# Kernel tuning notes

Hardware: AMD Instinct MI355X
Metric: run time of the kernel (lower is better)

Reference implementation:

```python
import jax, jax.numpy as jnp
import numpy as np

THRESHOLD = 0.5
NEG_POS_RATIO = 3
ALPHA = 10.0
N_PRIORS = 8732
N_CLASSES = 21
BATCH = 128
N_OBJ = 32


def cxcy_to_xy(cxcy):
    return jnp.concatenate([cxcy[..., :2] - cxcy[..., 2:] / 2.0,
                            cxcy[..., :2] + cxcy[..., 2:] / 2.0], axis=-1)


def xy_to_cxcy(xy):
    return jnp.concatenate([(xy[..., :2] + xy[..., 2:]) / 2.0,
                            xy[..., 2:] - xy[..., :2]], axis=-1)


def cxcy_to_gcxgcy(cxcy, priors_cxcy):
    return jnp.concatenate([(cxcy[..., :2] - priors_cxcy[..., :2]) / (priors_cxcy[..., 2:] / 10.0),
                            jnp.log(cxcy[..., 2:] / priors_cxcy[..., 2:]) * 5.0], axis=-1)


def find_jaccard_overlap(a, b):
    # a: (M,4) xyxy, b: (P,4) xyxy -> (M,P)
    lt = jnp.maximum(a[:, None, :2], b[None, :, :2])
    rb = jnp.minimum(a[:, None, 2:], b[None, :, 2:])
    wh = jnp.clip(rb - lt, 0.0)
    inter = wh[..., 0] * wh[..., 1]
    area_a = (a[:, 2] - a[:, 0]) * (a[:, 3] - a[:, 1])
    area_b = (b[:, 2] - b[:, 0]) * (b[:, 3] - b[:, 1])
    return inter / (area_a[:, None] + area_b[None, :] - inter)


def _match_one(boxes, labels, priors_xy, priors_cxcy):
    # boxes: (M,4) xyxy, labels: (M,)
    iou = find_jaccard_overlap(boxes, priors_xy)           # (M,P)
    obj_idx = jnp.argmax(iou, axis=1)                      # best prior per object
    iou = iou.at[jnp.arange(boxes.shape[0]), obj_idx].set(1.0)
    positive = (iou >= THRESHOLD).any(axis=0)              # (P,)
    max_prior_idx = jnp.argmax(iou, axis=0)                # best object per prior
    true_cls = labels[max_prior_idx] * positive.astype(labels.dtype)
    matched = boxes[max_prior_idx]                         # (P,4)
    true_locs = cxcy_to_gcxgcy(xy_to_cxcy(matched), priors_cxcy)
    return true_locs, true_cls, positive


def setup_inputs() -> dict:
    key = jax.random.key(0)
    k1, k2, k3, k4, k5, k6 = jax.random.split(key, 6)
    pred_loc = jax.random.normal(k1, (BATCH, N_PRIORS, 4), dtype=jnp.float32)
    pred_cls = jax.random.normal(k2, (BATCH, N_PRIORS, N_CLASSES), dtype=jnp.float32)
    # valid xyxy gt boxes in [0,1]
    p1 = jax.random.uniform(k3, (BATCH, N_OBJ, 2))
    p2 = jax.random.uniform(k4, (BATCH, N_OBJ, 2))
    b_boxes = jnp.concatenate([jnp.minimum(p1, p2), jnp.maximum(p1, p2) + 1e-3], axis=-1)
    b_boxes = jnp.clip(b_boxes, 0.0, 1.0).astype(jnp.float32)
    b_labels = jax.random.randint(k5, (BATCH, N_OBJ), 1, N_CLASSES)
    cxy = jax.random.uniform(k6, (N_PRIORS, 2), minval=0.1, maxval=0.9)
    wh = jax.random.uniform(jax.random.fold_in(k6, 1), (N_PRIORS, 2), minval=0.05, maxval=0.3)
    priors_cxcy = jnp.concatenate([cxy, wh], axis=-1).astype(jnp.float32)
    return {"pred_loc": pred_loc, "pred_cls": pred_cls, "b_boxes": b_boxes,
            "b_labels": b_labels, "priors_cxcy": priors_cxcy}


def reference(pred_loc, pred_cls, b_boxes, b_labels, priors_cxcy):
    batch_size, n_priors, n_classes = pred_cls.shape
    priors_xy = cxcy_to_xy(priors_cxcy)
    true_locs, true_classes, positive = jax.vmap(
        _match_one, in_axes=(0, 0, None, None))(b_boxes, b_labels, priors_xy, priors_cxcy)
    pos_f = positive.astype(pred_loc.dtype)                 # (B,P)
    n_positives = positive.sum(axis=1)                      # (B,)
    n_pos_total = n_positives.sum().astype(pred_loc.dtype)
    # L1 loss (mean over positive box elements)
    loc_loss = (jnp.abs(pred_loc - true_locs) * pos_f[..., None]).sum() / (n_pos_total * 4.0)
    # per-prior cross-entropy
    logp = jax.nn.log_softmax(pred_cls, axis=-1)
    ce = -jnp.take_along_axis(logp, true_classes[..., None], axis=-1)[..., 0]  # (B,P)
    conf_loss_pos = (ce * pos_f).sum()
    # hard negative mining: sort negatives descending per image
    conf_neg = jnp.where(positive, 0.0, ce)
    conf_neg_sorted = -jnp.sort(-conf_neg, axis=1)
    ranks = jnp.arange(n_priors)[None, :]
    hard_mask = ranks < (NEG_POS_RATIO * n_positives)[:, None]
    conf_loss_hard_neg = jnp.where(hard_mask, conf_neg_sorted, 0.0).sum()
    conf_loss = (conf_loss_hard_neg + conf_loss_pos) / n_pos_total
    loc_loss = ALPHA * loc_loss
    total_loss = conf_loss + loc_loss
    return total_loss, loc_loss, conf_loss
```

## Files before the change

### kernel.cpp

```cpp
#include <hip/hip_runtime.h>
#include <math.h>

#define B 128
#define M 32
#define P 8732
#define C 21
#define ALPHA 10.0f
#define NB2 35
#define CH 8
#define CS 1092

__global__ __launch_bounds__(256) void k1_partial(
    const float* __restrict__ b_boxes, const float* __restrict__ priors,
    float* __restrict__ pI, float* __restrict__ pU, int* __restrict__ pidx,
    int* __restrict__ done) {
  if (blockIdx.x == 0 && threadIdx.x == 0) *done = 0;
  int b = blockIdx.x >> 3;
  int ch = blockIdx.x & 7;
  int wid = threadIdx.x >> 6;
  int lane = threadIdx.x & 63;
  int obase = wid * 8;

  float ox1[8], oy1[8], ox2[8], oy2[8], oarea[8], bI[8], bU[8];
  int bidx[8];
#pragma unroll
  for (int k = 0; k < 8; k++) {
    float4 bx = ((const float4*)b_boxes)[(size_t)b * M + obase + k];
    ox1[k] = bx.x; oy1[k] = bx.y; ox2[k] = bx.z; oy2[k] = bx.w;
    oarea[k] = (bx.z - bx.x) * (bx.w - bx.y);
    bI[k] = -1.0f; bU[k] = 1.0f; bidx[k] = P;
  }

  int pend = (ch + 1) * CS;
  if (pend > P) pend = P;
#pragma unroll 2
  for (int p = ch * CS + lane; p < pend; p += 64) {
    float4 pr = ((const float4*)priors)[p];
    float pw2 = pr.z * 0.5f, ph2 = pr.w * 0.5f;
    float px1 = pr.x - pw2, py1 = pr.y - ph2;
    float px2 = pr.x + pw2, py2 = pr.y + ph2;
    float areaP = pr.z * pr.w;
#pragma unroll
    for (int k = 0; k < 8; k++) {
      float iw = fminf(ox2[k], px2) - fmaxf(ox1[k], px1);
      float ih = fminf(oy2[k], py2) - fmaxf(oy1[k], py1);
      iw = fmaxf(iw, 0.0f);
      ih = fmaxf(ih, 0.0f);
      float inter = iw * ih;
      float uni = oarea[k] + areaP - inter;
      if (inter * bU[k] > bI[k] * uni) { bI[k] = inter; bU[k] = uni; bidx[k] = p; }
    }
  }
  for (int off = 32; off >= 1; off >>= 1) {
#pragma unroll
    for (int k = 0; k < 8; k++) {
      float oI = __shfl_xor(bI[k], off, 64);
      float oU = __shfl_xor(bU[k], off, 64);
      int oi = __shfl_xor(bidx[k], off, 64);
      float l = oI * bU[k], r = bI[k] * oU;
      if (l > r || (l == r && oi < bidx[k])) { bI[k] = oI; bU[k] = oU; bidx[k] = oi; }
    }
  }
  if (lane == 0) {
#pragma unroll
    for (int k = 0; k < 8; k++) {
      int idx = ((size_t)b * M + obase + k) * CH + ch;
      pI[idx] = bI[k]; pU[idx] = bU[k]; pidx[idx] = bidx[k];
    }
  }
}

__global__ __launch_bounds__(1024) void k23_img(
    const float* __restrict__ pred_loc, const float* __restrict__ pred_cls,
    const float* __restrict__ b_boxes, const int* __restrict__ b_labels,
    const float* __restrict__ priors,
    const float* __restrict__ pI, const float* __restrict__ pU,
    const int* __restrict__ pidx,
    float* __restrict__ imgres, int* __restrict__ done,
    float* __restrict__ out) {
  int b = blockIdx.x;
  int tid = threadIdx.x;
  int wid = tid >> 6;
  int lane = tid & 63;

  __shared__ __align__(16) float s[P];
  __shared__ __align__(16) float4 sbox[M];
  __shared__ float sarea[M];
  __shared__ int slab[M], sobj[M];
  __shared__ float pl[NB2], pc[NB2];
  __shared__ int pn[NB2];
  __shared__ int histw[16 * 256];
  __shared__ __align__(16) int cnt[256];
  __shared__ int sdig, scum, sK, sLast;
  __shared__ float sLoc, sCe, sNp;
  __shared__ float rsum[16], rl[16], rc[16], rh[16], rn[16];
  __shared__ int rcnt[16];

  if (tid < M) {
    int m = tid;
    float4 bx = ((const float4*)b_boxes)[b * M + m];
    sbox[m] = bx;
    sarea[m] = (bx.z - bx.x) * (bx.w - bx.y);
    slab[m] = b_labels[b * M + m];
    int o = b * M + m;
    float cI = pI[o * CH], cU = pU[o * CH];
    int ci = pidx[o * CH];
#pragma unroll
    for (int ch = 1; ch < CH; ch++) {
      float nI = pI[o * CH + ch], nU = pU[o * CH + ch];
      int ni = pidx[o * CH + ch];
      if (nI * cU > cI * nU) { cI = nI; cU = nU; ci = ni; }
    }
    sobj[m] = ci;
  }
  __syncthreads();

  for (int x = wid; x < NB2; x += 16) {
    float accl = 0.0f, accc = 0.0f;
    int accn = 0;
    for (int w4 = 0; w4 < 4; w4++) {
      int p = x * 256 + w4 * 64 + lane;
      float locpart = 0.0f, cepospart = 0.0f;
      int npos = 0;
      if (p < P) {
        float4 pr = ((const float4*)priors)[p];
        float pw2 = pr.z * 0.5f, ph2 = pr.w * 0.5f;
        float px1 = pr.x - pw2, py1 = pr.y - ph2;
        float px2 = pr.x + pw2, py2 = pr.y + ph2;
        float areaP = pr.z * pr.w;
        float bI = -1.0f, bU = 1.0f;
        int bm = 0;
        int fm = 0x7fffffff;
        for (int m = 0; m < M; m++) {
          float4 bx = sbox[m];
          float iw = fminf(bx.z, px2) - fmaxf(bx.x, px1);
          float ih = fminf(bx.w, py2) - fmaxf(bx.y, py1);
          iw = fmaxf(iw, 0.0f);
          ih = fmaxf(ih, 0.0f);
          float inter = iw * ih;
          float uni = sarea[m] + areaP - inter;
          if (inter * bU > bI * uni) { bI = inter; bU = uni; bm = m; }
          if (fm == 0x7fffffff && sobj[m] == p) fm = m;
        }
        if (fm != 0x7fffffff) {
          if (!((bI == bU) && (bm < fm))) { bI = 1.0f; bU = 1.0f; bm = fm; }
        }
        bool pos = (2.0f * bI >= bU);
        int wAny = __any((int)pos);

        if (wAny) {
          float4 plv = ((const float4*)pred_loc)[(size_t)b * P + p];
          float4 bx = sbox[bm];
          float cx = (bx.x + bx.z) * 0.5f, cy = (bx.y + bx.w) * 0.5f;
          float w = bx.z - bx.x, h = bx.w - bx.y;
          float rz = __builtin_amdgcn_rcpf(pr.z);
          float rw = __builtin_amdgcn_rcpf(pr.w);
          float g0 = (cx - pr.x) * 10.0f * rz;
          float g1 = (cy - pr.y) * 10.0f * rw;
          float g2 = __logf(w * rz) * 5.0f;
          float g3 = __logf(h * rw) * 5.0f;
          if (pos) {
            locpart = fabsf(plv.x - g0) + fabsf(plv.y - g1) +
                      fabsf(plv.z - g2) + fabsf(plv.w - g3);
            npos = 1;
          }
        }

        const float* uu = pred_cls + ((size_t)b * P + p) * C;
        int cls = pos ? slab[bm] : 0;
        float se = 0.0f, vc = 0.0f;
#pragma unroll
        for (int c = 0; c < C; c++) {
          float xv = uu[c];
          se += __expf(xv);
          if (c == cls) vc = xv;
        }
        float ce = __logf(se) - vc;
        s[p] = pos ? 0.0f : ce;
        cepospart = pos ? ce : 0.0f;
      }
      for (int off = 32; off >= 1; off >>= 1) {
        locpart += __shfl_down(locpart, off, 64);
        cepospart += __shfl_down(cepospart, off, 64);
        npos += __shfl_down(npos, off, 64);
      }
      if (lane == 0) { accl += locpart; accc += cepospart; accn += npos; }
    }
    if (lane == 0) { pl[x] = accl; pc[x] = accc; pn[x] = accn; }
  }
  __syncthreads();

  if (wid == 0) {
    float lp = 0.0f, cp = 0.0f;
    int np = 0;
    if (lane < NB2) { lp = pl[lane]; cp = pc[lane]; np = pn[lane]; }
    for (int off = 32; off >= 1; off >>= 1) {
      lp += __shfl_down(lp, off, 64);
      cp += __shfl_down(cp, off, 64);
      np += __shfl_down(np, off, 64);
    }
    if (lane == 0) {
      int K = np * 3;
      if (K > P) K = P;
      sK = K; sLoc = lp; sCe = cp; sNp = (float)np;
    }
  }
  __syncthreads();

  int K = sK;
  unsigned pfx = 0;
  int Krem = K;
#pragma unroll
  for (int pass = 3; pass >= 0; --pass) {
    int sh = pass * 8;
    for (int i = tid; i < 16 * 256; i += 1024) histw[i] = 0;
    __syncthreads();
    unsigned himask = (pass == 3) ? 0u : (0xFFFFFFFFu << (sh + 8));
    int* myh = &histw[wid * 256];
    for (int i = tid; i < P; i += 1024) {
      unsigned ub = __float_as_uint(s[i]);
      if ((ub & himask) == pfx) atomicAdd(&myh[(ub >> sh) & 255], 1);
    }
    __syncthreads();
    if (tid < 256) {
      int c = 0;
#pragma unroll
      for (int w = 0; w < 16; w++) c += histw[w * 256 + tid];
      cnt[tid] = c;
    }
    __syncthreads();
    if (wid == 0) {
      int4 c4 = ((const int4*)cnt)[lane];
      int s3 = c4.w;
      int s2 = c4.z + s3;
      int s1 = c4.y + s2;
      int s0 = c4.x + s1;
      int suf = s0;
      for (int off = 1; off < 64; off <<= 1) {
        int t = __shfl_down(suf, off, 64);
        if (lane + off < 64) suf += t;
      }
      int above = suf - s0;
      int S0 = above + s0, S1 = above + s1, S2 = above + s2, S3 = above + s3;
      int S4 = above;
      if (S3 >= Krem && S4 < Krem) { sdig = 4 * lane + 3; scum = S4; }
      else if (S2 >= Krem && S3 < Krem) { sdig = 4 * lane + 2; scum = S3; }
      else if (S1 >= Krem && S2 < Krem) { sdig = 4 * lane + 1; scum = S2; }
      else if (S0 >= Krem && S1 < Krem) { sdig = 4 * lane + 0; scum = S1; }
    }
    __syncthreads();
    pfx |= ((unsigned)sdig) << sh;
    Krem -= scum;
  }
  float tau = __uint_as_float(pfx);

  float sum = 0.0f;
  int cgt = 0;
  for (int i = tid; i < P; i += 1024) {
    float v = s[i];
    if (v > tau) { sum += v; cgt++; }
  }
  for (int off = 32; off >= 1; off >>= 1) {
    sum += __shfl_down(sum, off, 64);
    cgt += __shfl_down(cgt, off, 64);
  }
  if (lane == 0) { rsum[wid] = sum; rcnt[wid] = cgt; }
  __syncthreads();
  if (tid == 0) {
    float stot = 0.0f;
    int ctot = 0;
#pragma unroll
    for (int w = 0; w < 16; w++) { stot += rsum[w]; ctot += rcnt[w]; }
    float hard = stot + (float)(K - ctot) * tau;
    imgres[b * 4 + 0] = sLoc;
    imgres[b * 4 + 1] = sCe;
    imgres[b * 4 + 2] = hard;
    imgres[b * 4 + 3] = sNp;
    __threadfence();
    int prev = atomicAdd(done, 1);
    sLast = (prev == B - 1) ? 1 : 0;
  }
  __syncthreads();
  if (sLast) {
    __threadfence();
    float l = 0.0f, c = 0.0f, h = 0.0f, n = 0.0f;
    if (tid < B) {
      l = atomicAdd(&imgres[tid * 4 + 0], 0.0f);
      c = atomicAdd(&imgres[tid * 4 + 1], 0.0f);
      h = atomicAdd(&imgres[tid * 4 + 2], 0.0f);
      n = atomicAdd(&imgres[tid * 4 + 3], 0.0f);
    }
    for (int off = 32; off >= 1; off >>= 1) {
      l += __shfl_down(l, off, 64);
      c += __shfl_down(c, off, 64);
      h += __shfl_down(h, off, 64);
      n += __shfl_down(n, off, 64);
    }
    if (lane == 0) { rl[wid] = l; rc[wid] = c; rh[wid] = h; rn[wid] = n; }
    __syncthreads();
    if (tid == 0) {
      float L = 0, Cc = 0, H = 0, N = 0;
#pragma unroll
      for (int w = 0; w < 16; w++) { L += rl[w]; Cc += rc[w]; H += rh[w]; N += rn[w]; }
      float loc = ALPHA * L / (N * 4.0f);
      float conf = (H + Cc) / N;
      out[0] = conf + loc;
      out[1] = loc;
      out[2] = conf;
    }
  }
}

extern "C" void kernel_launch(void* const* d_in, const int* in_sizes, int n_in,
                              void* d_out, int out_size, void* d_ws, size_t ws_size,
                              hipStream_t stream) {
  (void)in_sizes; (void)n_in; (void)out_size; (void)ws_size;
  const float* pred_loc = (const float*)d_in[0];
  const float* pred_cls = (const float*)d_in[1];
  const float* b_boxes = (const float*)d_in[2];
  const int* b_labels = (const int*)d_in[3];
  const float* priors = (const float*)d_in[4];
  float* out = (float*)d_out;

  int* done = (int*)d_ws;
  float* imgres = (float*)d_ws + 8;
  float* pI = imgres + B * 4;
  float* pU = pI + B * M * CH;
  int* pidx = (int*)(pU + B * M * CH);

  k1_partial<<<B * CH, 256, 0, stream>>>(b_boxes, priors, pI, pU, pidx, done);
  k23_img<<<B, 1024, 0, stream>>>(pred_loc, pred_cls, b_boxes, b_labels,
                                  priors, pI, pU, pidx, imgres, done, out);
}
```

Before: 246.9 us.

## Rebalance prior tiles across waves and register-block IoU over several tiles

The per-image phase now gives each wave 8 or 9 interleaved 64-prior subtiles instead of 2–3 chunks of 256 priors. This evens out work across the 16 waves. Each box is read from shared memory once per group of 4–5 subtiles held in registers, which raises ILP and cuts LDS traffic. The 21-class logits are loaded as unaligned float4 vectors instead of scalars. Partial sums go to a 140-entry array and are combined in groups of four, matching the old grouping. The costs are more registers per thread and a possible occupancy hit.

```diff
diff --git a/kernel.cpp b/kernel.cpp
--- a/kernel.cpp
+++ b/kernel.cpp
@@ -7,8 +7,14 @@
 #define C 21
 #define ALPHA 10.0f
 #define NB2 35
+#define NSUB 140
 #define CH 8
 #define CS 1092
+
+typedef float fx4 __attribute__((ext_vector_type(4)));
+typedef fx4 fx4u __attribute__((aligned(4)));
+
+#define CE1(val, idx) { float xv_ = (val); se += __expf(xv_); if (cls == (idx)) vc = xv_; }
 
 __global__ __launch_bounds__(256) void k1_partial(
     const float* __restrict__ b_boxes, const float* __restrict__ priors,
@@ -70,87 +76,67 @@
   }
 }
 
-__global__ __launch_bounds__(1024) void k23_img(
+template <int KN>
+__device__ __forceinline__ void phaseA_group(
+    int b, int wid, int lane, int koff, int ntw,
     const float* __restrict__ pred_loc, const float* __restrict__ pred_cls,
-    const float* __restrict__ b_boxes, const int* __restrict__ b_labels,
     const float* __restrict__ priors,
-    const float* __restrict__ pI, const float* __restrict__ pU,
-    const int* __restrict__ pidx,
-    float* __restrict__ imgres, int* __restrict__ done,
-    float* __restrict__ out) {
-  int b = blockIdx.x;
-  int tid = threadIdx.x;
-  int wid = tid >> 6;
-  int lane = tid & 63;
-
-  __shared__ __align__(16) float s[P];
-  __shared__ __align__(16) float4 sbox[M];
-  __shared__ float sarea[M];
-  __shared__ int slab[M], sobj[M];
-  __shared__ float pl[NB2], pc[NB2];
-  __shared__ int pn[NB2];
-  __shared__ int histw[16 * 256];
-  __shared__ __align__(16) int cnt[256];
-  __shared__ int sdig, scum, sK, sLast;
-  __shared__ float sLoc, sCe, sNp;
-  __shared__ float rsum[16], rl[16], rc[16], rh[16], rn[16];
-  __shared__ int rcnt[16];
-
-  if (tid < M) {
-    int m = tid;
-    float4 bx = ((const float4*)b_boxes)[b * M + m];
-    sbox[m] = bx;
-    sarea[m] = (bx.z - bx.x) * (bx.w - bx.y);
-    slab[m] = b_labels[b * M + m];
-    int o = b * M + m;
-    float cI = pI[o * CH], cU = pU[o * CH];
-    int ci = pidx[o * CH];
-#pragma unroll
-    for (int ch = 1; ch < CH; ch++) {
-      float nI = pI[o * CH + ch], nU = pU[o * CH + ch];
-      int ni = pidx[o * CH + ch];
-      if (nI * cU > cI * nU) { cI = nI; cU = nU; ci = ni; }
-    }
-    sobj[m] = ci;
-  }
-  __syncthreads();
-
-  for (int x = wid; x < NB2; x += 16) {
-    float accl = 0.0f, accc = 0.0f;
-    int accn = 0;
-    for (int w4 = 0; w4 < 4; w4++) {
-      int p = x * 256 + w4 * 64 + lane;
+    const float4* sbox, const int* slab, const int* sobj,
+    float* s, float* psl, float* psc, int* psn) {
+  float x1[KN], y1[KN], x2[KN], y2[KN], ap[KN];
+  float bIr[KN], bUr[KN];
+  int bmr[KN], fmr[KN];
+#pragma unroll
+  for (int j = 0; j < KN; j++) {
+    int k = koff + j;
+    int p = ((wid + (k << 4)) << 6) + lane;
+    x1[j] = 0.0f; y1[j] = 0.0f; x2[j] = 0.0f; y2[j] = 0.0f; ap[j] = 0.0f;
+    bIr[j] = -1.0f; bUr[j] = 1.0f; bmr[j] = 0; fmr[j] = 0x7fffffff;
+    if (k < ntw && p < P) {
+      float4 pr = ((const float4*)priors)[p];
+      float pw2 = pr.z * 0.5f, ph2 = pr.w * 0.5f;
+      x1[j] = pr.x - pw2; y1[j] = pr.y - ph2;
+      x2[j] = pr.x + pw2; y2[j] = pr.y + ph2;
+      ap[j] = pr.z * pr.w;
+    }
+  }
+  for (int m = 0; m < M; m++) {
+    float4 bx = sbox[m];
+    float areaB = (bx.z - bx.x) * (bx.w - bx.y);
+    int objm = sobj[m];
+#pragma unroll
+    for (int j = 0; j < KN; j++) {
+      float iw = fminf(bx.z, x2[j]) - fmaxf(bx.x, x1[j]);
+      float ih = fminf(bx.w, y2[j]) - fmaxf(bx.y, y1[j]);
+      iw = fmaxf(iw, 0.0f);
+      ih = fmaxf(ih, 0.0f);
+      float inter = iw * ih;
+      float uni = areaB + ap[j] - inter;
+      if (inter * bUr[j] > bIr[j] * uni) { bIr[j] = inter; bUr[j] = uni; bmr[j] = m; }
+      int p = ((wid + ((koff + j) << 4)) << 6) + lane;
+      if (fmr[j] == 0x7fffffff && objm == p) fmr[j] = m;
+    }
+  }
+#pragma unroll
+  for (int j = 0; j < KN; j++) {
+    int k = koff + j;
+    if (k < ntw) {
+      int t = wid + (k << 4);
+      int p = (t << 6) + lane;
       float locpart = 0.0f, cepospart = 0.0f;
       int npos = 0;
       if (p < P) {
-        float4 pr = ((const float4*)priors)[p];
-        float pw2 = pr.z * 0.5f, ph2 = pr.w * 0.5f;
-        float px1 = pr.x - pw2, py1 = pr.y - ph2;
-        float px2 = pr.x + pw2, py2 = pr.y + ph2;
-        float areaP = pr.z * pr.w;
-        float bI = -1.0f, bU = 1.0f;
-        int bm = 0;
-        int fm = 0x7fffffff;
-        for (int m = 0; m < M; m++) {
-          float4 bx = sbox[m];
-          float iw = fminf(bx.z, px2) - fmaxf(bx.x, px1);
-          float ih = fminf(bx.w, py2) - fmaxf(bx.y, py1);
-          iw = fmaxf(iw, 0.0f);
-          ih = fmaxf(ih, 0.0f);
-          float inter = iw * ih;
-          float uni = sarea[m] + areaP - inter;
-          if (inter * bU > bI * uni) { bI = inter; bU = uni; bm = m; }
-          if (fm == 0x7fffffff && sobj[m] == p) fm = m;
+        float bIv = bIr[j], bUv = bUr[j];
+        int bmv = bmr[j], fmv = fmr[j];
+        if (fmv != 0x7fffffff) {
+          if (!((bIv == bUv) && (bmv < fmv))) { bIv = 1.0f; bUv = 1.0f; bmv = fmv; }
         }
-        if (fm != 0x7fffffff) {
-          if (!((bI == bU) && (bm < fm))) { bI = 1.0f; bU = 1.0f; bm = fm; }
-        }
-        bool pos = (2.0f * bI >= bU);
+        bool pos = (2.0f * bIv >= bUv);
         int wAny = __any((int)pos);
-
         if (wAny) {
+          float4 pr = ((const float4*)priors)[p];
           float4 plv = ((const float4*)pred_loc)[(size_t)b * P + p];
-          float4 bx = sbox[bm];
+          float4 bx = sbox[bmv];
           float cx = (bx.x + bx.z) * 0.5f, cy = (bx.y + bx.w) * 0.5f;
           float w = bx.z - bx.x, h = bx.w - bx.y;
           float rz = __builtin_amdgcn_rcpf(pr.z);
@@ -165,16 +151,18 @@
             npos = 1;
           }
         }
-
+        int cls = pos ? slab[bmv] : 0;
         const float* uu = pred_cls + ((size_t)b * P + p) * C;
-        int cls = pos ? slab[bm] : 0;
+        const fx4u* u4 = (const fx4u*)uu;
+        fx4 a0 = u4[0], a1 = u4[1], a2 = u4[2], a3 = u4[3], a4 = u4[4];
+        float v20 = uu[20];
         float se = 0.0f, vc = 0.0f;
-#pragma unroll
-        for (int c = 0; c < C; c++) {
-          float xv = uu[c];
-          se += __expf(xv);
-          if (c == cls) vc = xv;
-        }
+        CE1(a0.x, 0)  CE1(a0.y, 1)  CE1(a0.z, 2)  CE1(a0.w, 3)
+        CE1(a1.x, 4)  CE1(a1.y, 5)  CE1(a1.z, 6)  CE1(a1.w, 7)
+        CE1(a2.x, 8)  CE1(a2.y, 9)  CE1(a2.z, 10) CE1(a2.w, 11)
+        CE1(a3.x, 12) CE1(a3.y, 13) CE1(a3.z, 14) CE1(a3.w, 15)
+        CE1(a4.x, 16) CE1(a4.y, 17) CE1(a4.z, 18) CE1(a4.w, 19)
+        CE1(v20, 20)
         float ce = __logf(se) - vc;
         s[p] = pos ? 0.0f : ce;
         cepospart = pos ? ce : 0.0f;
@@ -184,16 +172,70 @@
         cepospart += __shfl_down(cepospart, off, 64);
         npos += __shfl_down(npos, off, 64);
       }
-      if (lane == 0) { accl += locpart; accc += cepospart; accn += npos; }
-    }
-    if (lane == 0) { pl[x] = accl; pc[x] = accc; pn[x] = accn; }
-  }
+      if (lane == 0) { psl[t] = locpart; psc[t] = cepospart; psn[t] = npos; }
+    }
+  }
+}
+
+__global__ __launch_bounds__(1024) void k23_img(
+    const float* __restrict__ pred_loc, const float* __restrict__ pred_cls,
+    const float* __restrict__ b_boxes, const int* __restrict__ b_labels,
+    const float* __restrict__ priors,
+    const float* __restrict__ pI, const float* __restrict__ pU,
+    const int* __restrict__ pidx,
+    float* __restrict__ imgres, int* __restrict__ done,
+    float* __restrict__ out) {
+  int b = blockIdx.x;
+  int tid = threadIdx.x;
+  int wid = tid >> 6;
+  int lane = tid & 63;
+
+  __shared__ __align__(16) float s[P];
+  __shared__ __align__(16) float4 sbox[M];
+  __shared__ int slab[M], sobj[M];
+  __shared__ float psl[NSUB], psc[NSUB];
+  __shared__ int psn[NSUB];
+  __shared__ int histw[16 * 256];
+  __shared__ __align__(16) int cnt[256];
+  __shared__ int sdig, scum, sK, sLast;
+  __shared__ float sLoc, sCe, sNp;
+  __shared__ float rsum[16], rl[16], rc[16], rh[16], rn[16];
+  __shared__ int rcnt[16];
+
+  if (tid < M) {
+    int m = tid;
+    float4 bx = ((const float4*)b_boxes)[b * M + m];
+    sbox[m] = bx;
+    slab[m] = b_labels[b * M + m];
+    int o = b * M + m;
+    float cI = pI[o * CH], cU = pU[o * CH];
+    int ci = pidx[o * CH];
+#pragma unroll
+    for (int ch = 1; ch < CH; ch++) {
+      float nI = pI[o * CH + ch], nU = pU[o * CH + ch];
+      int ni = pidx[o * CH + ch];
+      if (nI * cU > cI * nU) { cI = nI; cU = nU; ci = ni; }
+    }
+    sobj[m] = ci;
+  }
+  __syncthreads();
+
+  int ntw = (wid < 12) ? 9 : 8;
+  phaseA_group<5>(b, wid, lane, 0, ntw, pred_loc, pred_cls, priors,
+                  sbox, slab, sobj, s, psl, psc, psn);
+  phaseA_group<4>(b, wid, lane, 5, ntw, pred_loc, pred_cls, priors,
+                  sbox, slab, sobj, s, psl, psc, psn);
   __syncthreads();
 
   if (wid == 0) {
     float lp = 0.0f, cp = 0.0f;
     int np = 0;
-    if (lane < NB2) { lp = pl[lane]; cp = pc[lane]; np = pn[lane]; }
+    if (lane < NB2) {
+      int t4 = lane * 4;
+      lp = ((psl[t4] + psl[t4 + 1]) + psl[t4 + 2]) + psl[t4 + 3];
+      cp = ((psc[t4] + psc[t4 + 1]) + psc[t4 + 2]) + psc[t4 + 3];
+      np = psn[t4] + psn[t4 + 1] + psn[t4 + 2] + psn[t4 + 3];
+    }
     for (int off = 32; off >= 1; off >>= 1) {
       lp += __shfl_down(lp, off, 64);
       cp += __shfl_down(cp, off, 64);
```

Measured after the change: 228.3 us. -7.5%, faster.
